# Kernel optimization log

Hardware: AMD Instinct MI355X
Metric: run time of the kernel (lower is better)

The kernel has to match this reference:

```python
import jax, jax.numpy as jnp
from jax import lax
import numpy as np

DN = ('NCHW', 'OIHW', 'NCHW')

def _leaky(x):
    return jnp.where(x > 0, x, 0.2 * x)

def _forward(texts, styles, conv1_w, conv1_b, conv2_w, conv2_b, proj_w, proj_b,
             v1_w, v1_b, v2_w, v2_b, v3_w, v3_b, d1_w, d1_b, d2_w, d2_b):
    bs, tot, W, H = texts.shape
    C = proj_w.shape[1]  # style_channels
    # stack text/style as 2-channel images: [bs*tot, 2, W, H]
    ts = jnp.stack((texts, styles), axis=2).reshape(bs * tot, 2, W, H)
    # transnet: conv -> leaky -> conv -> leaky -> GAP -> linear
    x = lax.conv_general_dilated(ts, conv1_w, (2, 2), 'SAME', dimension_numbers=DN)
    x = _leaky(x + conv1_b[None, :, None, None])
    x = lax.conv_general_dilated(x, conv2_w, (2, 2), 'SAME', dimension_numbers=DN)
    x = _leaky(x + conv2_b[None, :, None, None])
    x = x.mean(axis=(2, 3))                              # [bs*tot, 64]
    feats = (x @ proj_w + proj_b).reshape(bs, tot, C)     # [bs, tot, C]
    # vec2vec scorer MLP -> tanh score per option
    h = _leaky(feats @ v1_w + v1_b)
    h = _leaky(h @ v2_w + v2_b)
    score = jnp.tanh(h @ v3_w + v3_b)[..., 0]             # [bs, tot]
    # top-1 routing: argmax + gather of the selected style vector
    idx = jnp.argmax(score, axis=1)                       # [bs]
    res = jnp.take_along_axis(feats, idx[:, None, None], axis=1)[:, 0]  # [bs, C]
    # vec2im decoder: MLP -> image [bs, 1, W, H]
    img = jnp.tanh(_leaky(res @ d1_w + d1_b) @ d2_w + d2_b)
    return img.reshape(bs, 1, W, H)

def setup_inputs() -> dict:
    key = jax.random.key(0)
    ks = jax.random.split(key, 12)
    bs, tot, W, H = 32, 64, 64, 64
    C, C1, C2, NFC, DH = 128, 32, 64, 128, 512
    s = 0.05
    def rn(k, shape):
        return jax.random.normal(k, shape, dtype=jnp.float32) * s
    return {
        'texts': jax.random.normal(ks[0], (bs, tot, W, H), dtype=jnp.float32),
        'styles': jax.random.normal(ks[1], (bs, tot, W, H), dtype=jnp.float32),
        'conv1_w': rn(ks[2], (C1, 2, 3, 3)),
        'conv1_b': jnp.zeros((C1,), jnp.float32),
        'conv2_w': rn(ks[3], (C2, C1, 3, 3)),
        'conv2_b': jnp.zeros((C2,), jnp.float32),
        'proj_w': rn(ks[4], (C2, C)),
        'proj_b': jnp.zeros((C,), jnp.float32),
        'v1_w': rn(ks[5], (C, NFC)),
        'v1_b': jnp.zeros((NFC,), jnp.float32),
        'v2_w': rn(ks[6], (NFC, NFC)),
        'v2_b': jnp.zeros((NFC,), jnp.float32),
        'v3_w': rn(ks[7], (NFC, 1)),
        'v3_b': jnp.zeros((1,), jnp.float32),
        'd1_w': rn(ks[8], (C, DH)),
        'd1_b': jnp.zeros((DH,), jnp.float32),
        'd2_w': rn(ks[9], (DH, W * H)),
        'd2_b': jnp.zeros((W * H,), jnp.float32),
    }

def reference(texts, styles, conv1_w, conv1_b, conv2_w, conv2_b, proj_w, proj_b,
              v1_w, v1_b, v2_w, v2_b, v3_w, v3_b, d1_w, d1_b, d2_w, d2_b):
    return _forward(texts, styles, conv1_w, conv1_b, conv2_w, conv2_b, proj_w, proj_b,
                    v1_w, v1_b, v2_w, v2_b, v3_w, v3_b, d1_w, d1_b, d2_w, d2_b)
```

## Files before the change

### kernel.cpp

```cpp
#include <hip/hip_runtime.h>
#include <cstddef>
#include <cstdint>

#define LEAKY(x) ((x) > 0.f ? (x) : 0.2f*(x))

typedef _Float16 f16x8  __attribute__((ext_vector_type(8)));
typedef float    f32x4  __attribute__((ext_vector_type(4)));
typedef float    f32x16 __attribute__((ext_vector_type(16)));

#define WS_FEATS   0
#define WS_SCORES  262144
#define WS_W2      268288
#define WS_W1M     287744
#define WS_GAPP    288768

__global__ void kPack(const float* __restrict__ c1w, const float* __restrict__ c2w,
                      float* __restrict__ ws)
{
    _Float16* W2 = (_Float16*)(ws + WS_W2);
    _Float16* W1 = (_Float16*)(ws + WS_W1M);
    const int t = blockIdx.x*256 + threadIdx.x;
    for (int i = t; i < 2*64*152; i += 16*256) {
        int k = i % 152, rest = i / 152;
        int co = rest & 63, c = rest >> 6;
        _Float16 h = (_Float16)0.f, lo = (_Float16)0.f;
        if (k < 144) {
            int tap = k >> 4, cil = k & 15;
            float wv = c2w[(co*32 + c*16 + cil)*9 + tap];
            h  = (_Float16)wv;
            lo = (_Float16)(wv - (float)h);
        }
        W2[((size_t)(c*2 + 0)*64 + co)*152 + k] = h;
        W2[((size_t)(c*2 + 1)*64 + co)*152 + k] = lo;
    }
    if (t < 2048) {
        int pl = t >> 10, rest = t & 1023;
        int co = rest >> 5, k = rest & 31;
        int kh = k >> 3, j = k & 7, kw = j >> 1, ci = j & 1;
        float wv = 0.f;
        if (kh < 3 && kw < 3) wv = c1w[co*18 + ci*9 + kh*3 + kw];
        _Float16 hi = (_Float16)wv;
        W1[t] = pl ? (_Float16)(wv - (float)hi) : hi;
    }
}

__device__ __forceinline__ int x1_off(int pl, int hf, int row, int xp, int xq) {
    return (pl*2 + hf)*2528 + row*280 + (xp*17 + xq)*8;
}
#define X1_HALFS (2*2*2528)

__global__ __launch_bounds__(256, 4) void kConv(
    const float* __restrict__ texts, const float* __restrict__ styles,
    const float* __restrict__ c1b, const float* __restrict__ c2b,
    const float* __restrict__ wsro, float* __restrict__ gapp)
{
    __shared__ __align__(16) union {
        _Float16 in[2][19][68][2];
        float    part[4][32];
    } s_u;
    __shared__ __align__(16) _Float16 s_x1[X1_HALFS];

    const int bid = blockIdx.x, tid = threadIdx.x;
    const int n = bid >> 2, q = bid & 3;
    const int w = tid >> 6, l = tid & 63;

    {
        const uint4 z4 = {0u,0u,0u,0u};
        uint4* z = (uint4*)&s_x1[0];
        for (int i = tid; i < X1_HALFS/8; i += 256) z[i] = z4;
        if (tid < 38) {
            int pl = tid >= 19, row = pl ? tid - 19 : tid;
            *(uint4*)&s_u.in[pl][row][64][0] = z4;
        }
    }
    for (int u = tid; u < 304; u += 256) {
        const int row = u >> 4, g = u & 15;
        const int grow = q*16 + row;
        float4 tv = {0.f,0.f,0.f,0.f}, sv = {0.f,0.f,0.f,0.f};
        if (grow < 64) {
            tv = *(const float4*)&texts [(size_t)n*4096 + grow*64 + g*4];
            sv = *(const float4*)&styles[(size_t)n*4096 + grow*64 + g*4];
        }
        float vals[8] = {tv.x, sv.x, tv.y, sv.y, tv.z, sv.z, tv.w, sv.w};
        _Float16 hh[8], ll[8];
        #pragma unroll
        for (int j = 0; j < 8; ++j) {
            _Float16 hi = (_Float16)vals[j];
            hh[j] = hi; ll[j] = (_Float16)(vals[j] - (float)hi);
        }
        *(uint4*)&s_u.in[0][row][g*4][0] = *(uint4*)hh;
        *(uint4*)&s_u.in[1][row][g*4][0] = *(uint4*)ll;
    }
    __syncthreads();

    const _Float16* W2h = (const _Float16*)(wsro + WS_W2);
    const _Float16* W1g = (const _Float16*)(wsro + WS_W1M);

    f32x16 acc;
    #pragma unroll
    for (int r = 0; r < 16; ++r) acc[r] = 0.f;

    const int mt = w >> 1, nh = w & 1;
    const int posl = mt*32 + (l & 31);
    const int py2 = posl >> 4, px2 = posl & 15;
    const int hf2 = l >> 5;
    const int co2 = nh*32 + (l & 31);
    const int kg = l >> 4, m16 = l & 15;
    const int NT = (q == 3) ? 16 : 18;

    for (int ch = 0; ch < 2; ++ch) {
        {
            f16x8 a_h = *(const f16x8*)&W1g[(0*32 + ch*16 + m16)*32 + kg*8];
            f16x8 a_l = *(const f16x8*)&W1g[(1*32 + ch*16 + m16)*32 + kg*8];
            float4 b4 = *(const float4*)&c1b[ch*16 + kg*4];
            for (int t = w; t < NT; t += 4) {
                const int py = t >> 1, px = (t & 1)*16 + m16;
                const int row = (kg < 3) ? (2*py + kg) : (2*py);
                const _Float16* bp0 = &s_u.in[0][row][2*px][0];
                const _Float16* bp1 = &s_u.in[1][row][2*px][0];
                f16x8 b_h, b_l;
                ((uint2*)&b_h)[0] = *(const uint2*)bp0;
                ((uint2*)&b_h)[1] = *(const uint2*)(bp0 + 4);
                ((uint2*)&b_l)[0] = *(const uint2*)bp1;
                ((uint2*)&b_l)[1] = *(const uint2*)(bp1 + 4);
                f32x4 c = {0.f,0.f,0.f,0.f};
                c = __builtin_amdgcn_mfma_f32_16x16x32_f16(a_l, b_h, c, 0, 0, 0);
                c = __builtin_amdgcn_mfma_f32_16x16x32_f16(a_h, b_l, c, 0, 0, 0);
                c = __builtin_amdgcn_mfma_f32_16x16x32_f16(a_h, b_h, c, 0, 0, 0);
                const int xp = px & 1, xq = px >> 1;
                _Float16 hh[4], ll[4];
                #pragma unroll
                for (int r = 0; r < 4; ++r) {
                    float v = c[r] + b4[r];
                    v = fmaxf(v, 0.2f*v);
                    _Float16 hi = (_Float16)v;
                    hh[r] = hi; ll[r] = (_Float16)(v - (float)hi);
                }
                const int eo = (kg & 1)*4;
                *(uint2*)&s_x1[x1_off(0, kg >> 1, py, xp, xq) + eo] = *(uint2*)hh;
                *(uint2*)&s_x1[x1_off(1, kg >> 1, py, xp, xq) + eo] = *(uint2*)ll;
            }
        }
        __syncthreads();

        {
            const _Float16* Bg_h = W2h + ((size_t)(ch*2 + 0)*64 + co2)*152 + hf2*8;
            const _Float16* Bg_l = Bg_h + (size_t)64*152;
            #pragma unroll
            for (int tap = 0; tap < 9; ++tap) {
                const int kh = tap/3, kw = tap%3;
                const int xr = 2*px2 + kw;
                const int xp = xr & 1, xq = xr >> 1;
                const int r2 = 2*py2 + kh;
                f16x8 Ah = *(const f16x8*)&s_x1[x1_off(0, hf2, r2, xp, xq)];
                f16x8 Al = *(const f16x8*)&s_x1[x1_off(1, hf2, r2, xp, xq)];
                f16x8 Bh = *(const f16x8*)&Bg_h[tap*16];
                f16x8 Bl = *(const f16x8*)&Bg_l[tap*16];
                acc = __builtin_amdgcn_mfma_f32_32x32x16_f16(Ah, Bh, acc, 0, 0, 0);
                acc = __builtin_amdgcn_mfma_f32_32x32x16_f16(Al, Bh, acc, 0, 0, 0);
                acc = __builtin_amdgcn_mfma_f32_32x32x16_f16(Ah, Bl, acc, 0, 0, 0);
            }
        }
        __syncthreads();
    }

    {
        const float b2 = c2b[co2];
        float s = 0.f;
        #pragma unroll
        for (int r = 0; r < 16; ++r) {
            float v = acc[r] + b2;
            s += fmaxf(v, 0.2f*v);
        }
        s += __shfl_xor(s, 32);
        if (l < 32) s_u.part[w][l] = s;
    }
    __syncthreads();
    if (tid < 64) {
        const int nhc = tid >> 5, cl = tid & 31;
        float g = s_u.part[0*2 + nhc][cl] + s_u.part[1*2 + nhc][cl];
        gapp[(size_t)(n*4 + q)*64 + tid] = g;
    }
}

__global__ __launch_bounds__(128) void kScore(
    const float* __restrict__ gapp,
    const float* __restrict__ pw,  const float* __restrict__ pb,
    const float* __restrict__ v1w, const float* __restrict__ v1b,
    const float* __restrict__ v2w, const float* __restrict__ v2b,
    const float* __restrict__ v3w, const float* __restrict__ v3b,
    float* __restrict__ feats, float* __restrict__ scores)
{
    __shared__ float s_gap[64], s_f[128], s_h[128], s_red[2];
    const int n = blockIdx.x, tid = threadIdx.x;

    if (tid < 64) {
        const float* gp = &gapp[(size_t)n*256 + tid];
        s_gap[tid] = (gp[0] + gp[64] + gp[128] + gp[192]) * (1.f/256.f);
    }
    __syncthreads();
    {
        float a = pb[tid];
        #pragma unroll 8
        for (int m = 0; m < 64; ++m) a += s_gap[m]*pw[m*128 + tid];
        feats[(size_t)n*128 + tid] = a;
        s_f[tid] = a;
    }
    __syncthreads();
    {
        float a = v1b[tid];
        #pragma unroll 8
        for (int m = 0; m < 128; ++m) a += s_f[m]*v1w[m*128 + tid];
        s_h[tid] = LEAKY(a);
    }
    __syncthreads();
    {
        float a = v2b[tid];
        #pragma unroll 8
        for (int m = 0; m < 128; ++m) a += s_h[m]*v2w[m*128 + tid];
        a = LEAKY(a);
        s_f[tid] = a * v3w[tid];
    }
    __syncthreads();
    {
        float p = s_f[tid];
        #pragma unroll
        for (int off = 32; off; off >>= 1) p += __shfl_xor(p, off);
        if ((tid & 63) == 0) s_red[tid >> 6] = p;
    }
    __syncthreads();
    if (tid == 0) scores[n] = tanhf(s_red[0] + s_red[1] + v3b[0]);
}

__global__ __launch_bounds__(512) void kDecode(
    const float* __restrict__ scores, const float* __restrict__ feats,
    const float* __restrict__ d1w, const float* __restrict__ d1b,
    const float* __restrict__ d2w, const float* __restrict__ d2b,
    float* __restrict__ out)
{
    __shared__ float s_res[128];
    __shared__ float s_h[512];
    __shared__ int s_idx;
    const int bid = blockIdx.x;
    const int b = bid >> 3, ot = bid & 7;
    const int tid = threadIdx.x;

    if (tid < 64) {
        float v = scores[b*64 + tid];
        int   i = tid;
        #pragma unroll
        for (int off = 32; off; off >>= 1) {
            float ov = __shfl_xor(v, off);
            int   oi = __shfl_xor(i, off);
            if (ov > v || (ov == v && oi < i)) { v = ov; i = oi; }
        }
        if (tid == 0) s_idx = i;
    }
    __syncthreads();
    if (tid < 128) s_res[tid] = feats[((size_t)b*64 + s_idx)*128 + tid];
    __syncthreads();
    {
        float a = d1b[tid];
        #pragma unroll 8
        for (int m = 0; m < 128; ++m) a += s_res[m]*d1w[m*512 + tid];
        s_h[tid] = LEAKY(a);
    }
    __syncthreads();
    const int o = ot*512 + tid;
    float a = d2b[o];
    for (int k = 0; k < 512; k += 4) {
        float4 h4 = *(const float4*)&s_h[k];
        a += h4.x*d2w[(size_t)(k+0)*4096 + o];
        a += h4.y*d2w[(size_t)(k+1)*4096 + o];
        a += h4.z*d2w[(size_t)(k+2)*4096 + o];
        a += h4.w*d2w[(size_t)(k+3)*4096 + o];
    }
    out[(size_t)b*4096 + o] = tanhf(a);
}

extern "C" void kernel_launch(void* const* d_in, const int* in_sizes, int n_in,
                              void* d_out, int out_size, void* d_ws, size_t ws_size,
                              hipStream_t stream)
{
    const float* texts  = (const float*)d_in[0];
    const float* styles = (const float*)d_in[1];
    const float* c1w = (const float*)d_in[2];
    const float* c1b = (const float*)d_in[3];
    const float* c2w = (const float*)d_in[4];
    const float* c2b = (const float*)d_in[5];
    const float* pw  = (const float*)d_in[6];
    const float* pb  = (const float*)d_in[7];
    const float* v1w = (const float*)d_in[8];
    const float* v1b = (const float*)d_in[9];
    const float* v2w = (const float*)d_in[10];
    const float* v2b = (const float*)d_in[11];
    const float* v3w = (const float*)d_in[12];
    const float* v3b = (const float*)d_in[13];
    const float* d1w = (const float*)d_in[14];
    const float* d1b = (const float*)d_in[15];
    const float* d2w = (const float*)d_in[16];
    const float* d2b = (const float*)d_in[17];

    float* ws     = (float*)d_ws;
    float* feats  = ws + WS_FEATS;
    float* scores = ws + WS_SCORES;
    float* gapp   = ws + WS_GAPP;

    kPack<<<dim3(16), dim3(256), 0, stream>>>(c1w, c2w, ws);
    kConv<<<dim3(8192), dim3(256), 0, stream>>>(
        texts, styles, c1b, c2b, (const float*)ws, gapp);
    kScore<<<dim3(2048), dim3(128), 0, stream>>>(
        gapp, pw, pb, v1w, v1b, v2w, v2b, v3w, v3b, feats, scores);
    kDecode<<<dim3(256), dim3(512), 0, stream>>>(
        scores, feats, d1w, d1b, d2w, d2b, (float*)d_out);
}
```

Measured before the change: 140.8 us.

## Split conv1 channel halves across two wave groups in 512-thread conv blocks

The conv kernel now runs 512 threads per block. The two 16-channel halves of conv1 are handled at the same time by two groups of four waves, each writing its own shared-memory buffer, instead of looping over them one after another. Each group then runs its half of the conv2 reduction, and the partial accumulators are combined through shared memory before the bias, leaky activation and pooling. This removes one serial phase and two barriers per block and adds parallelism. In exchange it doubles the s_x1 shared-memory footprint, adds a cross-wave reduction, and drops the min-blocks launch bound, which may lower occupancy. The pack kernel grid also grows from 16 to 64 blocks.

```diff
diff --git a/kernel.cpp b/kernel.cpp
--- a/kernel.cpp
+++ b/kernel.cpp
@@ -20,7 +20,7 @@
     _Float16* W2 = (_Float16*)(ws + WS_W2);
     _Float16* W1 = (_Float16*)(ws + WS_W1M);
     const int t = blockIdx.x*256 + threadIdx.x;
-    for (int i = t; i < 2*64*152; i += 16*256) {
+    for (int i = t; i < 2*64*152; i += 64*256) {
         int k = i % 152, rest = i / 152;
         int co = rest & 63, c = rest >> 6;
         _Float16 h = (_Float16)0.f, lo = (_Float16)0.f;
@@ -49,7 +49,7 @@
 }
 #define X1_HALFS (2*2*2528)
 
-__global__ __launch_bounds__(256, 4) void kConv(
+__global__ __launch_bounds__(512) void kConv(
     const float* __restrict__ texts, const float* __restrict__ styles,
     const float* __restrict__ c1b, const float* __restrict__ c2b,
     const float* __restrict__ wsro, float* __restrict__ gapp)
@@ -58,7 +58,7 @@
         _Float16 in[2][19][68][2];
         float    part[4][32];
     } s_u;
-    __shared__ __align__(16) _Float16 s_x1[X1_HALFS];
+    __shared__ __align__(16) _Float16 s_x1[2][X1_HALFS];
 
     const int bid = blockIdx.x, tid = threadIdx.x;
     const int n = bid >> 2, q = bid & 3;
@@ -66,14 +66,14 @@
 
     {
         const uint4 z4 = {0u,0u,0u,0u};
-        uint4* z = (uint4*)&s_x1[0];
-        for (int i = tid; i < X1_HALFS/8; i += 256) z[i] = z4;
+        uint4* z = (uint4*)&s_x1[0][0];
+        for (int i = tid; i < 2*X1_HALFS/8; i += 512) z[i] = z4;
         if (tid < 38) {
             int pl = tid >= 19, row = pl ? tid - 19 : tid;
             *(uint4*)&s_u.in[pl][row][64][0] = z4;
         }
     }
-    for (int u = tid; u < 304; u += 256) {
+    for (int u = tid; u < 304; u += 512) {
         const int row = u >> 4, g = u & 15;
         const int grow = q*16 + row;
         float4 tv = {0.f,0.f,0.f,0.f}, sv = {0.f,0.f,0.f,0.f};
@@ -100,7 +100,8 @@
     #pragma unroll
     for (int r = 0; r < 16; ++r) acc[r] = 0.f;
 
-    const int mt = w >> 1, nh = w & 1;
+    const int ck = w >> 2, sw = w & 3;
+    const int mt = (w >> 1) & 1, nh = w & 1;
     const int posl = mt*32 + (l & 31);
     const int py2 = posl >> 4, px2 = posl & 15;
     const int hf2 = l >> 5;
@@ -108,68 +109,75 @@
     const int kg = l >> 4, m16 = l & 15;
     const int NT = (q == 3) ? 16 : 18;
 
-    for (int ch = 0; ch < 2; ++ch) {
-        {
-            f16x8 a_h = *(const f16x8*)&W1g[(0*32 + ch*16 + m16)*32 + kg*8];
-            f16x8 a_l = *(const f16x8*)&W1g[(1*32 + ch*16 + m16)*32 + kg*8];
-            float4 b4 = *(const float4*)&c1b[ch*16 + kg*4];
-            for (int t = w; t < NT; t += 4) {
-                const int py = t >> 1, px = (t & 1)*16 + m16;
-                const int row = (kg < 3) ? (2*py + kg) : (2*py);
-                const _Float16* bp0 = &s_u.in[0][row][2*px][0];
-                const _Float16* bp1 = &s_u.in[1][row][2*px][0];
-                f16x8 b_h, b_l;
-                ((uint2*)&b_h)[0] = *(const uint2*)bp0;
-                ((uint2*)&b_h)[1] = *(const uint2*)(bp0 + 4);
-                ((uint2*)&b_l)[0] = *(const uint2*)bp1;
-                ((uint2*)&b_l)[1] = *(const uint2*)(bp1 + 4);
-                f32x4 c = {0.f,0.f,0.f,0.f};
-                c = __builtin_amdgcn_mfma_f32_16x16x32_f16(a_l, b_h, c, 0, 0, 0);
-                c = __builtin_amdgcn_mfma_f32_16x16x32_f16(a_h, b_l, c, 0, 0, 0);
-                c = __builtin_amdgcn_mfma_f32_16x16x32_f16(a_h, b_h, c, 0, 0, 0);
-                const int xp = px & 1, xq = px >> 1;
-                _Float16 hh[4], ll[4];
-                #pragma unroll
-                for (int r = 0; r < 4; ++r) {
-                    float v = c[r] + b4[r];
-                    v = fmaxf(v, 0.2f*v);
-                    _Float16 hi = (_Float16)v;
-                    hh[r] = hi; ll[r] = (_Float16)(v - (float)hi);
-                }
-                const int eo = (kg & 1)*4;
-                *(uint2*)&s_x1[x1_off(0, kg >> 1, py, xp, xq) + eo] = *(uint2*)hh;
-                *(uint2*)&s_x1[x1_off(1, kg >> 1, py, xp, xq) + eo] = *(uint2*)ll;
+    {
+        f16x8 a_h = *(const f16x8*)&W1g[(0*32 + ck*16 + m16)*32 + kg*8];
+        f16x8 a_l = *(const f16x8*)&W1g[(1*32 + ck*16 + m16)*32 + kg*8];
+        float4 b4 = *(const float4*)&c1b[ck*16 + kg*4];
+        for (int t = sw; t < NT; t += 4) {
+            const int py = t >> 1, px = (t & 1)*16 + m16;
+            const int row = (kg < 3) ? (2*py + kg) : (2*py);
+            const _Float16* bp0 = &s_u.in[0][row][2*px][0];
+            const _Float16* bp1 = &s_u.in[1][row][2*px][0];
+            f16x8 b_h, b_l;
+            ((uint2*)&b_h)[0] = *(const uint2*)bp0;
+            ((uint2*)&b_h)[1] = *(const uint2*)(bp0 + 4);
+            ((uint2*)&b_l)[0] = *(const uint2*)bp1;
+            ((uint2*)&b_l)[1] = *(const uint2*)(bp1 + 4);
+            f32x4 c = {0.f,0.f,0.f,0.f};
+            c = __builtin_amdgcn_mfma_f32_16x16x32_f16(a_l, b_h, c, 0, 0, 0);
+            c = __builtin_amdgcn_mfma_f32_16x16x32_f16(a_h, b_l, c, 0, 0, 0);
+            c = __builtin_amdgcn_mfma_f32_16x16x32_f16(a_h, b_h, c, 0, 0, 0);
+            const int xp = px & 1, xq = px >> 1;
+            _Float16 hh[4], ll[4];
+            #pragma unroll
+            for (int r = 0; r < 4; ++r) {
+                float v = c[r] + b4[r];
+                v = fmaxf(v, 0.2f*v);
+                _Float16 hi = (_Float16)v;
+                hh[r] = hi; ll[r] = (_Float16)(v - (float)hi);
             }
-        }
-        __syncthreads();
-
-        {
-            const _Float16* Bg_h = W2h + ((size_t)(ch*2 + 0)*64 + co2)*152 + hf2*8;
-            const _Float16* Bg_l = Bg_h + (size_t)64*152;
-            #pragma unroll
-            for (int tap = 0; tap < 9; ++tap) {
-                const int kh = tap/3, kw = tap%3;
-                const int xr = 2*px2 + kw;
-                const int xp = xr & 1, xq = xr >> 1;
-                const int r2 = 2*py2 + kh;
-                f16x8 Ah = *(const f16x8*)&s_x1[x1_off(0, hf2, r2, xp, xq)];
-                f16x8 Al = *(const f16x8*)&s_x1[x1_off(1, hf2, r2, xp, xq)];
-                f16x8 Bh = *(const f16x8*)&Bg_h[tap*16];
-                f16x8 Bl = *(const f16x8*)&Bg_l[tap*16];
-                acc = __builtin_amdgcn_mfma_f32_32x32x16_f16(Ah, Bh, acc, 0, 0, 0);
-                acc = __builtin_amdgcn_mfma_f32_32x32x16_f16(Al, Bh, acc, 0, 0, 0);
-                acc = __builtin_amdgcn_mfma_f32_32x32x16_f16(Ah, Bl, acc, 0, 0, 0);
-            }
-        }
-        __syncthreads();
-    }
-
-    {
+            const int eo = (kg & 1)*4;
+            *(uint2*)&s_x1[ck][x1_off(0, kg >> 1, py, xp, xq) + eo] = *(uint2*)hh;
+            *(uint2*)&s_x1[ck][x1_off(1, kg >> 1, py, xp, xq) + eo] = *(uint2*)ll;
+        }
+    }
+    __syncthreads();
+
+    {
+        const _Float16* Bg_h = W2h + ((size_t)(ck*2 + 0)*64 + co2)*152 + hf2*8;
+        const _Float16* Bg_l = Bg_h + (size_t)64*152;
+        #pragma unroll
+        for (int tap = 0; tap < 9; ++tap) {
+            const int kh = tap/3, kw = tap%3;
+            const int xr = 2*px2 + kw;
+            const int xp = xr & 1, xq = xr >> 1;
+            const int r2 = 2*py2 + kh;
+            f16x8 Ah = *(const f16x8*)&s_x1[ck][x1_off(0, hf2, r2, xp, xq)];
+            f16x8 Al = *(const f16x8*)&s_x1[ck][x1_off(1, hf2, r2, xp, xq)];
+            f16x8 Bh = *(const f16x8*)&Bg_h[tap*16];
+            f16x8 Bl = *(const f16x8*)&Bg_l[tap*16];
+            acc = __builtin_amdgcn_mfma_f32_32x32x16_f16(Ah, Bh, acc, 0, 0, 0);
+            acc = __builtin_amdgcn_mfma_f32_32x32x16_f16(Al, Bh, acc, 0, 0, 0);
+            acc = __builtin_amdgcn_mfma_f32_32x32x16_f16(Ah, Bl, acc, 0, 0, 0);
+        }
+    }
+    __syncthreads();
+
+    float* comb = (float*)&s_x1[0][0];
+    if (ck == 1) {
+        float* dst = comb + ((w - 4)*64 + l)*18;
+        #pragma unroll
+        for (int r = 0; r < 16; r += 2)
+            *(float2*)&dst[r] = make_float2(acc[r], acc[r+1]);
+    }
+    __syncthreads();
+    if (ck == 0) {
+        const float* src = comb + (w*64 + l)*18;
         const float b2 = c2b[co2];
         float s = 0.f;
         #pragma unroll
         for (int r = 0; r < 16; ++r) {
-            float v = acc[r] + b2;
+            float v = acc[r] + src[r] + b2;
             s += fmaxf(v, 0.2f*v);
         }
         s += __shfl_xor(s, 32);
@@ -306,8 +314,8 @@
     float* scores = ws + WS_SCORES;
     float* gapp   = ws + WS_GAPP;
 
-    kPack<<<dim3(16), dim3(256), 0, stream>>>(c1w, c2w, ws);
-    kConv<<<dim3(8192), dim3(256), 0, stream>>>(
+    kPack<<<dim3(64), dim3(256), 0, stream>>>(c1w, c2w, ws);
+    kConv<<<dim3(8192), dim3(512), 0, stream>>>(
         texts, styles, c1b, c2b, (const float*)ws, gapp);
     kScore<<<dim3(2048), dim3(128), 0, stream>>>(
         gapp, pw, pb, v1w, v1b, v2w, v2b, v3w, v3b, feats, scores);
```

New measurement: 141.3 us. About the same (+0.3%).
